# Optimization experiments

Hardware: AMD Instinct MI355X
Metric: run time of the kernel (lower is better)

Reference implementation:

```python
import jax, jax.numpy as jnp
import numpy as np

BLOCK = 128          # fp8 quantization block size (from linear_deepseek_v3)
FP8_MAX = 448.0      # max representable value of float8_e4m3fn
F8 = jnp.float8_e4m3fn
G, T, K, N = 8, 1024, 7168, 2048


def setup_inputs() -> dict:
    key = jax.random.key(0)
    kx, kw, kb = jax.random.split(key, 3)
    xs = jax.random.normal(kx, (G, T, K), jnp.float32)
    # Build an fp8 block-quantized weight + per-(128x128)-block fp32 scale,
    # matching the stored self.weight (fp8) and self.scale parameters.
    w_raw = jax.random.normal(kw, (G, N, K), jnp.float32)
    wb = w_raw.reshape(G, N // BLOCK, BLOCK, K // BLOCK, BLOCK)
    amax = jnp.max(jnp.abs(wb), axis=(2, 4))            # [G, NB, KB]
    scale = amax / FP8_MAX
    w_q = (wb / scale[:, :, None, :, None]).astype(F8).astype(jnp.float32)
    weight = w_q.reshape(G, N, K)                        # fp8 code values held in fp32
    bias = jax.random.normal(kb, (G, N), jnp.float32) * 0.02
    return {"xs": xs, "weight": weight, "scale": scale, "bias": bias}


def reference(xs, weight, scale, bias):
    """Grouped fp8 block-quantized GEMM with inline dequant.
    xs:     [G, T, K] fp32 activations (one slab per group)
    weight: [G, N, K] fp8-quantized weights (stored as fp32 code values)
    scale:  [G, N/128, K/128] fp32 per-block weight scales
    bias:   [G, N] fp32
    """
    g, t, k = xs.shape
    n = weight.shape[1]
    kb, nb = k // BLOCK, n // BLOCK
    # --- act_quant_deepseek_v3: per (token, 128-col block) absmax/448 scale ---
    xb = xs.reshape(g, t, kb, BLOCK)
    a_scale = jnp.max(jnp.abs(xb), axis=-1) / FP8_MAX        # [G, T, KB]
    x_q = (xb / a_scale[..., None]).astype(F8).astype(jnp.float32)
    x_deq = (x_q * a_scale[..., None]).reshape(g, t, k)      # fused dequant
    # --- weight dequant: broadcast per-(128x128)-block scale ---
    w_deq = (weight.reshape(g, nb, BLOCK, kb, BLOCK)
             * scale[:, :, None, :, None]).reshape(g, n, k)
    # --- grouped GEMM (y = x A^T) + bias, fp32 accumulation ---
    y = jnp.einsum('gtk,gnk->gtn', x_deq, w_deq) + bias[:, None, :]
    return y
```

## Files before the change

kernel.cpp:

```cpp
#include <hip/hip_runtime.h>
#include <hip/hip_bf16.h>
#include <stdint.h>

#define G_ 8
#define T_ 1024
#define K_ 7168
#define N_ 2048
#define KB_ 56
#define NB_ 16
#define NT8_ 56

#define ACT_WGS  57344
#define WREC_WGS 28672

typedef __attribute__((ext_vector_type(4))) float f32x4;
typedef __attribute__((ext_vector_type(8))) int   i32x8;

typedef __attribute__((address_space(3))) uint32_t lds_u32_t;
typedef const __attribute__((address_space(1))) uint32_t gbl_u32_t;

__device__ __forceinline__ void gload_lds16(const void* gsrc, const void* ldst)
{
    __builtin_amdgcn_global_load_lds(
        (gbl_u32_t*)(uintptr_t)gsrc,
        (lds_u32_t*)(uint32_t)(uintptr_t)ldst, 16, 0, 0);
}

__device__ __forceinline__ void blockbar()
{
    asm volatile("" ::: "memory");
    __builtin_amdgcn_s_barrier();
    asm volatile("" ::: "memory");
}

__global__ __launch_bounds__(256) void prep_kernel(
    const float* __restrict__ xs, uint8_t* __restrict__ xq8,
    float* __restrict__ ascale,
    const float* __restrict__ w, uint8_t* __restrict__ wq8)
{
    const int bid = blockIdx.x;
    const int tid = threadIdx.x;
    if (bid < ACT_WGS) {
        const int grp = (bid * 256 + tid) >> 5;
        const int l   = tid & 31;
        const size_t base = (size_t)grp * 128 + (size_t)l * 4;

        const float4 v = *(const float4*)(xs + base);
        float am = fmaxf(fmaxf(fabsf(v.x), fabsf(v.y)),
                         fmaxf(fabsf(v.z), fabsf(v.w)));
#pragma unroll
        for (int off = 1; off <= 16; off <<= 1)
            am = fmaxf(am, __shfl_xor(am, off, 64));

        const float rs = 448.0f / am;
        const float s  = am * (1.0f / 448.0f);

        int pk = __builtin_amdgcn_cvt_pk_fp8_f32(v.x * rs, v.y * rs, 0, false);
        pk     = __builtin_amdgcn_cvt_pk_fp8_f32(v.z * rs, v.w * rs, pk, true);
        *(uint32_t*)(xq8 + base) = (uint32_t)pk;

        if (l == 0) {
            const int kb = grp % KB_;
            const int t  = (grp / KB_) & (T_ - 1);
            const int g  = grp / (KB_ * T_);
            ascale[(((size_t)(g * 4 + (t >> 8))) * KB_ + kb) * 256 + (t & 255)] = s;
        }
    } else {
        const size_t i = ((size_t)(bid - ACT_WGS) * 256 + tid) * 16;
        uint32_t o[4];
#pragma unroll
        for (int q = 0; q < 4; ++q) {
            const float4 a = *(const float4*)(w + i + q * 4);
            int pk = __builtin_amdgcn_cvt_pk_fp8_f32(a.x, a.y, 0, false);
            pk     = __builtin_amdgcn_cvt_pk_fp8_f32(a.z, a.w, pk, true);
            o[q] = (uint32_t)pk;
        }
        *(uint4*)(wq8 + i) = make_uint4(o[0], o[1], o[2], o[3]);
    }
}

union Frag { i32x8 v; struct { int4 lo, hi; } p; };

#define RD_FRAG(dst, base, r)                                                 \
  { const int rx_ = ((r) & 7) << 4;                                           \
    const char* bp_ = smem + (base) + (r)*128;                                \
    dst.p.lo = *(const int4*)(bp_ + ((lhi*32) ^ rx_));                        \
    dst.p.hi = *(const int4*)(bp_ + ((lhi*32 + 16) ^ rx_)); }

#define STG_A(c, t, bb) gload_lds16(pA8[c] + (size_t)(t)*128,                 \
      smem + (bb)*16384 + (c)*4096 + ptid*16)
#define STG_B(c, t, bb) gload_lds16(pB8[c] + (size_t)(t)*128,                 \
      smem + 65536 + (bb)*16384 + (c)*4096 + ptid*16)
#define STG_S(c) gload_lds16(pS + (size_t)(c)*2048,                           \
      smem + 131072 + ((c)&1)*4096 + ptid*16)

__global__ __launch_bounds__(512, 1) void gemm_fp8_kernel(
    const uint8_t* __restrict__ xq8, const uint8_t* __restrict__ wq8,
    const float* __restrict__ ascale, const float* __restrict__ wscale,
    const float* __restrict__ bias, float* __restrict__ y)
{
    __shared__ char smem[139520];

    const int bx0 = blockIdx.x;
    const int g     = bx0 & 7;
    const int inner = bx0 >> 3;
    const int tm    = inner & 7;
    const int tn    = inner >> 3;
    const int t0 = tm * 128, n0 = tn * 128;

    const int tid  = threadIdx.x, lane = tid & 63, wid = tid >> 6;
    const bool producer = (wid >= 4);
    const int ptid = tid & 255;
    const int l15 = lane & 15, lhi = lane >> 4;
    const int wrow = (wid >> 1) * 64;
    const int wcol = (wid & 1) * 64;

    const uint8_t* Ag = xq8 + (size_t)g * T_ * K_;
    const uint8_t* Bg = wq8 + (size_t)g * N_ * K_;

    const int srow = ptid >> 3;
    const int xoff = ((ptid & 7) ^ (srow & 7)) * 16;
    const uint8_t* pA8[4];
    const uint8_t* pB8[4];
#pragma unroll
    for (int c = 0; c < 4; ++c) {
        pA8[c] = Ag + (size_t)(t0 + c * 32 + srow) * K_ + xoff;
        pB8[c] = Bg + (size_t)(n0 + c * 32 + srow) * K_ + xoff;
    }
    const float* pS = ascale + ((size_t)(g * 4 + (tm >> 1)) * KB_) * 256
                    + (ptid >> 5) * 256 + (tm & 1) * 128 + (ptid & 31) * 4;

    const f32x4 z4 = {0.f, 0.f, 0.f, 0.f};
    f32x4 acc[4][4] = {};
    Frag bF[4];
    f32x4 asv[4];

    if (producer) {
        if (ptid < KB_) {
            const float wv = wscale[((size_t)(g * NB_ + tn)) * KB_ + ptid];
            *(float*)(smem + 139264 + ptid * 4) = wv;
        }
        STG_S(0);
#pragma unroll
        for (int c = 0; c < 4; ++c) { STG_A(c, 0, 0); STG_B(c, 0, 0); }
#pragma unroll
        for (int c = 0; c < 4; ++c) { STG_A(c, 1, 1); STG_B(c, 1, 1); }
#pragma unroll
        for (int c = 0; c < 4; ++c) { STG_A(c, 2, 2); STG_B(c, 2, 2); }
        asm volatile("s_waitcnt vmcnt(16)" ::: "memory");
        asm volatile("s_waitcnt lgkmcnt(0)" ::: "memory");
    } else {
        __builtin_amdgcn_s_setprio(1);
    }
    blockbar();

    int cur = 0;
    for (int u = 0; u < NT8_; ++u) {
        const int sbuf = (u >> 3) & 1;

        if (producer) {
            if ((u & 7) == 0 && u + 8 < NT8_) STG_S((u >> 3) + 1);
            if (u + 3 < NT8_) {
                const int fb = (cur + 3) & 3;
#pragma unroll
                for (int c = 0; c < 4; ++c) { STG_A(c, u + 3, fb); STG_B(c, u + 3, fb); }
                asm volatile("s_waitcnt vmcnt(16)" ::: "memory");
            } else if (u + 2 < NT8_) {
                asm volatile("s_waitcnt vmcnt(8)" ::: "memory");
            } else if (u + 1 < NT8_) {
                asm volatile("s_waitcnt vmcnt(0)" ::: "memory");
            }
        } else {
            const float wsc = *(const float*)(smem + 139264 + u * 4);
            const int abase = cur * 16384;
            const int bbase = 65536 + cur * 16384;

#pragma unroll
            for (int n = 0; n < 4; ++n)
                RD_FRAG(bF[n], bbase, wcol + n * 16 + l15);
#pragma unroll
            for (int m = 0; m < 4; ++m) {
                const float4 sv = *(const float4*)(smem + 131072 + sbuf * 4096 +
                    (u & 7) * 512 + (wrow + m * 16 + lhi * 4) * 4);
                asv[m][0] = sv.x * wsc; asv[m][1] = sv.y * wsc;
                asv[m][2] = sv.z * wsc; asv[m][3] = sv.w * wsc;
            }

#pragma unroll
            for (int m = 0; m < 4; ++m) {
                Frag aF;
                RD_FRAG(aF, abase, wrow + m * 16 + l15);
#pragma unroll
                for (int n = 0; n < 4; ++n) {
                    f32x4 blk = __builtin_amdgcn_mfma_scale_f32_16x16x128_f8f6f4(
                        aF.v, bF[n].v, z4, 0, 0, 0, 0x7F7F7F7F, 0, 0x7F7F7F7F);
                    acc[m][n] += blk * asv[m];
                }
            }
        }

        blockbar();
        cur = (cur + 1) & 3;
    }

    if (!producer) {
        float* Yg = y + (size_t)g * T_ * N_;
#pragma unroll
        for (int n = 0; n < 4; ++n) {
            const int col = n0 + wcol + n * 16 + l15;
            const float bv = bias[g * N_ + col];
#pragma unroll
            for (int m = 0; m < 4; ++m) {
                const int r0 = t0 + wrow + m * 16 + lhi * 4;
#pragma unroll
                for (int j = 0; j < 4; ++j)
                    Yg[(size_t)(r0 + j) * N_ + col] = acc[m][n][j] + bv;
            }
        }
    }
}

extern "C" void kernel_launch(void* const* d_in, const int* in_sizes, int n_in,
                              void* d_out, int out_size, void* d_ws, size_t ws_size,
                              hipStream_t stream)
{
    const float* xs     = (const float*)d_in[0];
    const float* weight = (const float*)d_in[1];
    const float* scale  = (const float*)d_in[2];
    const float* bias   = (const float*)d_in[3];
    float* y = (float*)d_out;

    uint8_t* xq8  = (uint8_t*)d_ws;
    float*   ascl = (float*)((char*)d_ws + 58720256);
    uint8_t* wq8  = (uint8_t*)((char*)d_ws + 60555264);

    prep_kernel<<<ACT_WGS + WREC_WGS, 256, 0, stream>>>(
        xs, xq8, ascl, weight, wq8);

    gemm_fp8_kernel<<<G_ * (T_ / 128) * (N_ / 128), 512, 0, stream>>>(
        xq8, wq8, ascl, scale, bias, y);
}
```

Before: 332.7 us.

## Make GEMM persistent over four M-tiles and process two K-steps per barrier

The GEMM launch shrinks from 1024 workgroups to 256, one per CU, and each workgroup loops over four M-tiles that share the same N-tile and group. The inner loop now consumes two K-steps per block barrier, with the producer issuing two stages at a time and waiting for all loads to finish. The aim is to remove the wave-quantization tail and halve the barrier count, possibly with better L2 reuse of the weight tile. In exchange, prefetch depth drops from three stages to a drain-to-zero pattern, which can expose load latency, and each tile change adds a pipeline refill.

```diff
diff --git a/kernel.cpp b/kernel.cpp
--- a/kernel.cpp
+++ b/kernel.cpp
@@ -9,6 +9,7 @@
 #define KB_ 56
 #define NB_ 16
 #define NT8_ 56
+#define NV_ 28
 
 #define ACT_WGS  57344
 #define WREC_WGS 28672
@@ -104,9 +105,9 @@
     const int bx0 = blockIdx.x;
     const int g     = bx0 & 7;
     const int inner = bx0 >> 3;
-    const int tm    = inner & 7;
-    const int tn    = inner >> 3;
-    const int t0 = tm * 128, n0 = tn * 128;
+    const int tn    = inner >> 1;
+    const int jj    = inner & 1;
+    const int n0    = tn * 128;
 
     const int tid  = threadIdx.x, lane = tid & 63, wid = tid >> 6;
     const bool producer = (wid >= 4);
@@ -120,18 +121,12 @@
 
     const int srow = ptid >> 3;
     const int xoff = ((ptid & 7) ^ (srow & 7)) * 16;
-    const uint8_t* pA8[4];
     const uint8_t* pB8[4];
 #pragma unroll
-    for (int c = 0; c < 4; ++c) {
-        pA8[c] = Ag + (size_t)(t0 + c * 32 + srow) * K_ + xoff;
+    for (int c = 0; c < 4; ++c)
         pB8[c] = Bg + (size_t)(n0 + c * 32 + srow) * K_ + xoff;
-    }
-    const float* pS = ascale + ((size_t)(g * 4 + (tm >> 1)) * KB_) * 256
-                    + (ptid >> 5) * 256 + (tm & 1) * 128 + (ptid & 31) * 4;
 
     const f32x4 z4 = {0.f, 0.f, 0.f, 0.f};
-    f32x4 acc[4][4] = {};
     Frag bF[4];
     f32x4 asv[4];
 
@@ -140,81 +135,98 @@
             const float wv = wscale[((size_t)(g * NB_ + tn)) * KB_ + ptid];
             *(float*)(smem + 139264 + ptid * 4) = wv;
         }
-        STG_S(0);
-#pragma unroll
-        for (int c = 0; c < 4; ++c) { STG_A(c, 0, 0); STG_B(c, 0, 0); }
-#pragma unroll
-        for (int c = 0; c < 4; ++c) { STG_A(c, 1, 1); STG_B(c, 1, 1); }
-#pragma unroll
-        for (int c = 0; c < 4; ++c) { STG_A(c, 2, 2); STG_B(c, 2, 2); }
-        asm volatile("s_waitcnt vmcnt(16)" ::: "memory");
-        asm volatile("s_waitcnt lgkmcnt(0)" ::: "memory");
     } else {
         __builtin_amdgcn_s_setprio(1);
     }
-    blockbar();
-
-    int cur = 0;
-    for (int u = 0; u < NT8_; ++u) {
-        const int sbuf = (u >> 3) & 1;
+
+    for (int tt = 0; tt < 4; ++tt) {
+        const int tm = jj + 2 * tt;
+        const int t0 = tm * 128;
+
+        const uint8_t* pA8[4];
+#pragma unroll
+        for (int c = 0; c < 4; ++c)
+            pA8[c] = Ag + (size_t)(t0 + c * 32 + srow) * K_ + xoff;
+        const float* pS = ascale + ((size_t)(g * 4 + (tm >> 1)) * KB_) * 256
+                        + (ptid >> 5) * 256 + (tm & 1) * 128 + (ptid & 31) * 4;
+
+        f32x4 acc[4][4] = {};
 
         if (producer) {
-            if ((u & 7) == 0 && u + 8 < NT8_) STG_S((u >> 3) + 1);
-            if (u + 3 < NT8_) {
-                const int fb = (cur + 3) & 3;
-#pragma unroll
-                for (int c = 0; c < 4; ++c) { STG_A(c, u + 3, fb); STG_B(c, u + 3, fb); }
-                asm volatile("s_waitcnt vmcnt(16)" ::: "memory");
-            } else if (u + 2 < NT8_) {
-                asm volatile("s_waitcnt vmcnt(8)" ::: "memory");
-            } else if (u + 1 < NT8_) {
+            STG_S(0);
+#pragma unroll
+            for (int c = 0; c < 4; ++c) { STG_A(c, 0, 0); STG_B(c, 0, 0); }
+#pragma unroll
+            for (int c = 0; c < 4; ++c) { STG_A(c, 1, 1); STG_B(c, 1, 1); }
+            asm volatile("s_waitcnt vmcnt(0)" ::: "memory");
+            asm volatile("s_waitcnt lgkmcnt(0)" ::: "memory");
+        }
+        blockbar();
+
+        for (int v = 0; v < NV_; ++v) {
+            if (producer) {
+                if ((v & 3) == 0 && 2 * v + 8 < NT8_) STG_S((v >> 2) + 1);
+                const int w0 = 2 * v + 2;
+                if (w0 < NT8_) {
+                    const int b0 = w0 & 3, b1 = (w0 + 1) & 3;
+#pragma unroll
+                    for (int c = 0; c < 4; ++c) { STG_A(c, w0, b0); STG_B(c, w0, b0); }
+#pragma unroll
+                    for (int c = 0; c < 4; ++c) { STG_A(c, w0 + 1, b1); STG_B(c, w0 + 1, b1); }
+                }
                 asm volatile("s_waitcnt vmcnt(0)" ::: "memory");
-            }
-        } else {
-            const float wsc = *(const float*)(smem + 139264 + u * 4);
-            const int abase = cur * 16384;
-            const int bbase = 65536 + cur * 16384;
-
-#pragma unroll
-            for (int n = 0; n < 4; ++n)
-                RD_FRAG(bF[n], bbase, wcol + n * 16 + l15);
-#pragma unroll
-            for (int m = 0; m < 4; ++m) {
-                const float4 sv = *(const float4*)(smem + 131072 + sbuf * 4096 +
-                    (u & 7) * 512 + (wrow + m * 16 + lhi * 4) * 4);
-                asv[m][0] = sv.x * wsc; asv[m][1] = sv.y * wsc;
-                asv[m][2] = sv.z * wsc; asv[m][3] = sv.w * wsc;
-            }
-
-#pragma unroll
-            for (int m = 0; m < 4; ++m) {
-                Frag aF;
-                RD_FRAG(aF, abase, wrow + m * 16 + l15);
-#pragma unroll
-                for (int n = 0; n < 4; ++n) {
-                    f32x4 blk = __builtin_amdgcn_mfma_scale_f32_16x16x128_f8f6f4(
-                        aF.v, bF[n].v, z4, 0, 0, 0, 0x7F7F7F7F, 0, 0x7F7F7F7F);
-                    acc[m][n] += blk * asv[m];
+            } else {
+#pragma unroll
+                for (int ks = 0; ks < 2; ++ks) {
+                    const int u = 2 * v + ks;
+                    const int buf = u & 3;
+                    const int sbuf = (u >> 3) & 1;
+                    const float wsc = *(const float*)(smem + 139264 + u * 4);
+                    const int abase = buf * 16384;
+                    const int bbase = 65536 + buf * 16384;
+
+#pragma unroll
+                    for (int n = 0; n < 4; ++n)
+                        RD_FRAG(bF[n], bbase, wcol + n * 16 + l15);
+#pragma unroll
+                    for (int m = 0; m < 4; ++m) {
+                        const float4 sv = *(const float4*)(smem + 131072 +
+                            sbuf * 4096 + (u & 7) * 512 +
+                            (wrow + m * 16 + lhi * 4) * 4);
+                        asv[m][0] = sv.x * wsc; asv[m][1] = sv.y * wsc;
+                        asv[m][2] = sv.z * wsc; asv[m][3] = sv.w * wsc;
+                    }
+#pragma unroll
+                    for (int m = 0; m < 4; ++m) {
+                        Frag aF;
+                        RD_FRAG(aF, abase, wrow + m * 16 + l15);
+#pragma unroll
+                        for (int n = 0; n < 4; ++n) {
+                            f32x4 blk =
+                                __builtin_amdgcn_mfma_scale_f32_16x16x128_f8f6f4(
+                                    aF.v, bF[n].v, z4, 0, 0,
+                                    0, 0x7F7F7F7F, 0, 0x7F7F7F7F);
+                            acc[m][n] += blk * asv[m];
+                        }
+                    }
                 }
             }
-        }
-
-        blockbar();
-        cur = (cur + 1) & 3;
-    }
-
-    if (!producer) {
-        float* Yg = y + (size_t)g * T_ * N_;
-#pragma unroll
-        for (int n = 0; n < 4; ++n) {
-            const int col = n0 + wcol + n * 16 + l15;
-            const float bv = bias[g * N_ + col];
-#pragma unroll
-            for (int m = 0; m < 4; ++m) {
-                const int r0 = t0 + wrow + m * 16 + lhi * 4;
-#pragma unroll
-                for (int j = 0; j < 4; ++j)
-                    Yg[(size_t)(r0 + j) * N_ + col] = acc[m][n][j] + bv;
+            blockbar();
+        }
+
+        if (!producer) {
+            float* Yg = y + (size_t)g * T_ * N_;
+#pragma unroll
+            for (int n = 0; n < 4; ++n) {
+                const int col = n0 + wcol + n * 16 + l15;
+                const float bv = bias[g * N_ + col];
+#pragma unroll
+                for (int m = 0; m < 4; ++m) {
+                    const int r0 = t0 + wrow + m * 16 + lhi * 4;
+#pragma unroll
+                    for (int j = 0; j < 4; ++j)
+                        Yg[(size_t)(r0 + j) * N_ + col] = acc[m][n][j] + bv;
+                }
             }
         }
     }
@@ -237,6 +249,6 @@
     prep_kernel<<<ACT_WGS + WREC_WGS, 256, 0, stream>>>(
         xs, xq8, ascl, weight, wq8);
 
-    gemm_fp8_kernel<<<G_ * (T_ / 128) * (N_ / 128), 512, 0, stream>>>(
+    gemm_fp8_kernel<<<256, 512, 0, stream>>>(
         xq8, wq8, ascl, scale, bias, y);
 }
```

After: 362.8 us. +9.1%, slower.
